# Kernel tuning notes

Measured on AMD Instinct MI355X. Metric: run time of the kernel, lower is better.

## Reference

```python
import jax, jax.numpy as jnp
import numpy as np

EPS = 1e-5

def _conv(x, w, stride=1, padding=0):
    return jax.lax.conv_general_dilated(
        x, w, window_strides=(stride, stride),
        padding=((padding, padding), (padding, padding)),
        dimension_numbers=('NCHW', 'OIHW', 'NCHW'))

def _bn(x, gamma, beta, mean, var):
    # inference-mode batchnorm, per-channel over NCHW
    inv = gamma / jnp.sqrt(var + EPS)
    return x * inv[None, :, None, None] + (beta - mean * inv)[None, :, None, None]

def setup_inputs() -> dict:
    key = jax.random.key(0)
    ks = jax.random.split(key, 16)
    B, Cin, H, W = 64, 1024, 28, 28
    width, Cout = 256, 1024
    d = {}
    d['x'] = jax.random.normal(ks[0], (B, Cin, H, W), jnp.float32)
    d['w1'] = jax.random.normal(ks[1], (width, Cin, 1, 1), jnp.float32) * 0.03
    d['w2'] = jax.random.normal(ks[2], (width, width, 3, 3), jnp.float32) * 0.02
    d['w3'] = jax.random.normal(ks[3], (Cout, width, 1, 1), jnp.float32) * 0.03
    for i, c in [(1, width), (2, width), (3, Cout)]:
        d[f'g{i}'] = jnp.ones((c,), jnp.float32)
        d[f'b{i}'] = jnp.zeros((c,), jnp.float32)
        d[f'm{i}'] = jax.random.normal(ks[4 + i], (c,), jnp.float32) * 0.1
        d[f'v{i}'] = jax.random.uniform(ks[8 + i], (c,), jnp.float32, 0.5, 1.5)
    return d

def reference(x, w1, w2, w3, g1, b1, m1, v1, g2, b2, m2, v2, g3, b3, m3, v3):
    out = jax.nn.relu(_bn(_conv(x, w1), g1, b1, m1, v1))
    out = jax.nn.relu(_bn(_conv(out, w2, stride=1, padding=1), g2, b2, m2, v2))
    out = _bn(_conv(out, w3), g3, b3, m3, v3)
    return jax.nn.relu(out + x)
```

## Files before the change

kernel.cpp:

```cpp
#include <hip/hip_runtime.h>
#include <hip/hip_bf16.h>
#include <cstdint>
#include <cstddef>

#define EPS_BN 1e-5f
#define LDK 40
#define TILE (128 * LDK)

typedef __attribute__((ext_vector_type(8))) __bf16 bf16x8;
typedef __attribute__((ext_vector_type(4))) float f32x4;

__device__ __forceinline__ unsigned short f2b(float f) {
    __hip_bfloat16 h = __float2bfloat16(f);
    return __builtin_bit_cast(unsigned short, h);
}
__device__ __forceinline__ unsigned int pack2(float a, float b) {
    return (unsigned int)f2b(a) | ((unsigned int)f2b(b) << 16);
}
__device__ __forceinline__ void lgkm_barrier() {
    __builtin_amdgcn_s_waitcnt(0xC07F);
    __builtin_amdgcn_s_barrier();
}


__global__ void prep_bn_kernel(const float* __restrict__ g1, const float* __restrict__ b1,
                               const float* __restrict__ m1, const float* __restrict__ v1,
                               const float* __restrict__ g2, const float* __restrict__ b2,
                               const float* __restrict__ m2, const float* __restrict__ v2,
                               const float* __restrict__ g3, const float* __restrict__ b3,
                               const float* __restrict__ m3, const float* __restrict__ v3,
                               float* __restrict__ bias1, float* __restrict__ bias2,
                               float* __restrict__ bias3) {
    int t = blockIdx.x * 256 + threadIdx.x;
    if (t < 256) {
        float inv = g1[t] * rsqrtf(v1[t] + EPS_BN);
        bias1[t] = b1[t] - m1[t] * inv;
    } else if (t < 512) {
        int c = t - 256;
        float inv = g2[c] * rsqrtf(v2[c] + EPS_BN);
        bias2[c] = b2[c] - m2[c] * inv;
    } else if (t < 1536) {
        int c = t - 512;
        float inv = g3[c] * rsqrtf(v3[c] + EPS_BN);
        bias3[c] = b3[c] - m3[c] * inv;
    }
}

__global__ void repack_w1(const float* __restrict__ w1, const float* __restrict__ g1,
                          const float* __restrict__ v1, unsigned short* __restrict__ w1b) {
    int idx = blockIdx.x * 256 + threadIdx.x;
    int co = idx >> 10;
    float inv = g1[co] * rsqrtf(v1[co] + EPS_BN);
    w1b[idx] = f2b(w1[idx] * inv);
}

__global__ void repack_w2(const float* __restrict__ w2, const float* __restrict__ g2,
                          const float* __restrict__ v2, unsigned short* __restrict__ w2r) {
    int idx = blockIdx.x * 256 + threadIdx.x;
    int k9 = idx >> 16;
    int rem = idx & 65535;
    int co = rem >> 8;
    int ci = rem & 255;
    float inv = g2[co] * rsqrtf(v2[co] + EPS_BN);
    w2r[idx] = f2b(w2[(co * 256 + ci) * 9 + k9] * inv);
}

__global__ void repack_w3(const float* __restrict__ w3, const float* __restrict__ g3,
                          const float* __restrict__ v3, unsigned short* __restrict__ w3b) {
    int idx = blockIdx.x * 256 + threadIdx.x;
    int co = idx >> 8;
    float inv = g3[co] * rsqrtf(v3[co] + EPS_BN);
    w3b[idx] = f2b(w3[idx] * inv);
}

__global__ void halo_zero(unsigned short* __restrict__ in2p) {
    int idx = blockIdx.x * 256 + threadIdx.x;
    int cell = idx >> 5, l8 = idx & 31;
    int n = cell / 116, c = cell % 116;
    int h, w;
    if (c < 30)      { h = 0;      w = c; }
    else if (c < 60) { h = 29;     w = c - 30; }
    else if (c < 88) { h = c - 59; w = 0; }
    else             { h = c - 87; w = 29; }
    uint4 z = {0u, 0u, 0u, 0u};
    *reinterpret_cast<uint4*>(in2p + (((size_t)n * 900) + h * 30 + w) * 256 + l8 * 8) = z;
}

__global__ __launch_bounds__(256) void transpose_x(const float* __restrict__ x,
                                                   unsigned short* __restrict__ xt) {
    __shared__ float t[64][65];
    const int tid = threadIdx.x;
    const int sp0 = blockIdx.x * 64;
    const int c0 = blockIdx.y * 64;
    const int n = blockIdx.z;
    const float* xn = x + (size_t)n * 1024 * 784;

#pragma unroll
    for (int it = 0; it < 4; ++it) {
        int ci = it * 16 + (tid >> 4);
        int spl = (tid & 15) * 4;
        int sp = sp0 + spl;
        float4 v = {0.f, 0.f, 0.f, 0.f};
        if (sp < 784) v = *reinterpret_cast<const float4*>(xn + (size_t)(c0 + ci) * 784 + sp);
        t[ci][spl + 0] = v.x;
        t[ci][spl + 1] = v.y;
        t[ci][spl + 2] = v.z;
        t[ci][spl + 3] = v.w;
    }
    __syncthreads();

    unsigned short* xtn = xt + (size_t)n * 784 * 1024;
#pragma unroll
    for (int it = 0; it < 2; ++it) {
        int spl = it * 32 + (tid >> 3);
        int sp = sp0 + spl;
        if (sp >= 784) continue;
        int ci8 = (tid & 7) * 8;
        float v0 = t[ci8 + 0][spl], v1 = t[ci8 + 1][spl];
        float v2 = t[ci8 + 2][spl], v3 = t[ci8 + 3][spl];
        float v4 = t[ci8 + 4][spl], v5 = t[ci8 + 5][spl];
        float v6 = t[ci8 + 6][spl], v7 = t[ci8 + 7][spl];
        uint4 o = {pack2(v0, v1), pack2(v2, v3), pack2(v4, v5), pack2(v6, v7)};
        *reinterpret_cast<uint4*>(xtn + (size_t)sp * 1024 + c0 + ci8) = o;
    }
}

__device__ __forceinline__ void mfma_step(const unsigned short* As, const unsigned short* Bs,
                                          int aoff, int boff, f32x4 acc[4][4]) {
    bf16x8 a[4], b[4];
#pragma unroll
    for (int i = 0; i < 4; ++i)
        a[i] = *reinterpret_cast<const bf16x8*>(As + aoff + i * 16 * LDK);
#pragma unroll
    for (int j = 0; j < 4; ++j)
        b[j] = *reinterpret_cast<const bf16x8*>(Bs + boff + j * 16 * LDK);
#pragma unroll
    for (int i = 0; i < 4; ++i)
#pragma unroll
        for (int j = 0; j < 4; ++j)
            acc[i][j] = __builtin_amdgcn_mfma_f32_16x16x32_bf16(a[i], b[j], acc[i][j], 0, 0, 0);
}

__global__ __launch_bounds__(256) void conv1_kernel(const unsigned short* __restrict__ xt,
                                                    const unsigned short* __restrict__ w1b,
                                                    const float* __restrict__ bias1,
                                                    unsigned short* __restrict__ in2p) {
    __shared__ unsigned short As[2][TILE];
    __shared__ unsigned short Bs[2][TILE];
    const int tid = threadIdx.x;
    const int f0 = blockIdx.x * 128;
    const int m0 = blockIdx.y * 128;
    const int lane = tid & 63, wave = tid >> 6;
    const int wr = wave >> 1, wc = wave & 1;
    const int l15 = lane & 15, quad = lane >> 4;
    const int tcid = tid & 3, tcl = tid >> 2;

    const unsigned short* aptr = w1b + (size_t)(m0 + tcl) * 1024 + tcid * 8;
    const unsigned short* bptr = xt + (size_t)(f0 + tcl) * 1024 + tcid * 8;

    f32x4 acc[4][4] = {};
    const int aoff = (wr * 64 + l15) * LDK + quad * 8;
    const int boff = (wc * 64 + l15) * LDK + quad * 8;
    const int wo = tcl * LDK + tcid * 8;

    uint4 ra0, ra1, rb0, rb1;
    ra0 = *reinterpret_cast<const uint4*>(aptr);
    ra1 = *reinterpret_cast<const uint4*>(aptr + 65536);
    rb0 = *reinterpret_cast<const uint4*>(bptr);
    rb1 = *reinterpret_cast<const uint4*>(bptr + 65536);

    for (int kk = 0; kk < 32; ++kk) {
        unsigned short* A = As[kk & 1];
        unsigned short* B = Bs[kk & 1];
        *reinterpret_cast<uint4*>(A + wo) = ra0;
        *reinterpret_cast<uint4*>(A + 64 * LDK + wo) = ra1;
        *reinterpret_cast<uint4*>(B + wo) = rb0;
        *reinterpret_cast<uint4*>(B + 64 * LDK + wo) = rb1;
        if (kk < 31) {
            int k0 = (kk + 1) * 32;
            ra0 = *reinterpret_cast<const uint4*>(aptr + k0);
            ra1 = *reinterpret_cast<const uint4*>(aptr + 65536 + k0);
            rb0 = *reinterpret_cast<const uint4*>(bptr + k0);
            rb1 = *reinterpret_cast<const uint4*>(bptr + 65536 + k0);
        }
        lgkm_barrier();
        mfma_step(A, B, aoff, boff, acc);
    }

#pragma unroll
    for (int j = 0; j < 4; ++j) {
        int f = f0 + wc * 64 + j * 16 + l15;
        int n = f / 784;
        int r = f - n * 784;
        int oh = r / 28, ow = r - oh * 28;
        unsigned short* dst = in2p + ((size_t)n * 900 + (oh + 1) * 30 + (ow + 1)) * 256;
#pragma unroll
        for (int i = 0; i < 4; ++i) {
            int co = m0 + wr * 64 + i * 16 + quad * 4;
            float4 bia = *reinterpret_cast<const float4*>(bias1 + co);
            f32x4 v = acc[i][j];
            ushort4 o;
            o.x = f2b(fmaxf(v.x + bia.x, 0.f));
            o.y = f2b(fmaxf(v.y + bia.y, 0.f));
            o.z = f2b(fmaxf(v.z + bia.z, 0.f));
            o.w = f2b(fmaxf(v.w + bia.w, 0.f));
            *reinterpret_cast<ushort4*>(dst + co) = o;
        }
    }
}

__global__ __launch_bounds__(256) void conv2_kernel(const unsigned short* __restrict__ in2p,
                                                    const unsigned short* __restrict__ w2r,
                                                    const float* __restrict__ bias2,
                                                    unsigned short* __restrict__ in3) {
    __shared__ unsigned short As[2][TILE];
    __shared__ unsigned short Bs[2][TILE];
    const int tid = threadIdx.x;
    const int f0 = blockIdx.x * 128;
    const int m0 = blockIdx.y * 128;
    const int lane = tid & 63, wave = tid >> 6;
    const int wr = wave >> 1, wc = wave & 1;
    const int l15 = lane & 15, quad = lane >> 4;
    const int tcid = tid & 3, tcl = tid >> 2;

    int cellc[2];
#pragma unroll
    for (int p = 0; p < 2; ++p) {
        int f = f0 + p * 64 + tcl;
        int n = f / 784;
        int r = f - n * 784;
        int oh = r / 28, ow = r - oh * 28;
        cellc[p] = n * 900 + (oh + 1) * 30 + (ow + 1);
    }

    f32x4 acc[4][4] = {};
    const int aoff = (wr * 64 + l15) * LDK + quad * 8;
    const int boff = (wc * 64 + l15) * LDK + quad * 8;
    const int wo = tcl * LDK + tcid * 8;

    uint4 ra0, ra1, rb0, rb1;
    {
        const unsigned short* wb = w2r;
        ra0 = *reinterpret_cast<const uint4*>(wb + (size_t)(m0 + tcl) * 256 + tcid * 8);
        ra1 = *reinterpret_cast<const uint4*>(wb + (size_t)(m0 + 64 + tcl) * 256 + tcid * 8);
        int dd = -31;
        rb0 = *reinterpret_cast<const uint4*>(in2p + (size_t)(cellc[0] + dd) * 256 + tcid * 8);
        rb1 = *reinterpret_cast<const uint4*>(in2p + (size_t)(cellc[1] + dd) * 256 + tcid * 8);
    }

    for (int kk = 0; kk < 72; ++kk) {
        unsigned short* A = As[kk & 1];
        unsigned short* B = Bs[kk & 1];
        *reinterpret_cast<uint4*>(A + wo) = ra0;
        *reinterpret_cast<uint4*>(A + 64 * LDK + wo) = ra1;
        *reinterpret_cast<uint4*>(B + wo) = rb0;
        *reinterpret_cast<uint4*>(B + 64 * LDK + wo) = rb1;
        if (kk < 71) {
            int kn = kk + 1;
            int k9 = kn >> 3, cb = kn & 7;
            int kh = k9 / 3, kw = k9 - 3 * kh;
            int dd = (kh - 1) * 30 + (kw - 1);
            const unsigned short* wb = w2r + (size_t)k9 * 65536 + cb * 32;
            ra0 = *reinterpret_cast<const uint4*>(wb + (size_t)(m0 + tcl) * 256 + tcid * 8);
            ra1 = *reinterpret_cast<const uint4*>(wb + (size_t)(m0 + 64 + tcl) * 256 + tcid * 8);
            const unsigned short* bb = in2p + (size_t)cb * 32 + tcid * 8;
            rb0 = *reinterpret_cast<const uint4*>(bb + (size_t)(cellc[0] + dd) * 256);
            rb1 = *reinterpret_cast<const uint4*>(bb + (size_t)(cellc[1] + dd) * 256);
        }
        lgkm_barrier();
        mfma_step(A, B, aoff, boff, acc);
    }

#pragma unroll
    for (int j = 0; j < 4; ++j) {
        int f = f0 + wc * 64 + j * 16 + l15;
        unsigned short* dst = in3 + (size_t)f * 256;
#pragma unroll
        for (int i = 0; i < 4; ++i) {
            int co = m0 + wr * 64 + i * 16 + quad * 4;
            float4 bia = *reinterpret_cast<const float4*>(bias2 + co);
            f32x4 v = acc[i][j];
            ushort4 o;
            o.x = f2b(fmaxf(v.x + bia.x, 0.f));
            o.y = f2b(fmaxf(v.y + bia.y, 0.f));
            o.z = f2b(fmaxf(v.z + bia.z, 0.f));
            o.w = f2b(fmaxf(v.w + bia.w, 0.f));
            *reinterpret_cast<ushort4*>(dst + co) = o;
        }
    }
}

__global__ __launch_bounds__(256) void conv3_kernel(const unsigned short* __restrict__ in3,
                                                    const unsigned short* __restrict__ w3b,
                                                    const float* __restrict__ bias3,
                                                    const float* __restrict__ x,
                                                    float* __restrict__ out) {
    __shared__ unsigned short As[2][TILE];
    __shared__ unsigned short Bs[2][TILE];
    const int tid = threadIdx.x;
    const int f0 = blockIdx.x * 128;
    const int m0 = blockIdx.y * 128;
    const int lane = tid & 63, wave = tid >> 6;
    const int wr = wave >> 1, wc = wave & 1;
    const int l15 = lane & 15, quad = lane >> 4;
    const int tcid = tid & 3, tcl = tid >> 2;

    const unsigned short* aptr = in3 + (size_t)(f0 + tcl) * 256 + tcid * 8;
    const unsigned short* bptr = w3b + (size_t)(m0 + tcl) * 256 + tcid * 8;

    f32x4 acc[4][4] = {};
    const int aoff = (wr * 64 + l15) * LDK + quad * 8;
    const int boff = (wc * 64 + l15) * LDK + quad * 8;
    const int wo = tcl * LDK + tcid * 8;

    uint4 ra0, ra1, rb0, rb1;
    ra0 = *reinterpret_cast<const uint4*>(aptr);
    ra1 = *reinterpret_cast<const uint4*>(aptr + 16384);
    rb0 = *reinterpret_cast<const uint4*>(bptr);
    rb1 = *reinterpret_cast<const uint4*>(bptr + 16384);

    for (int kk = 0; kk < 8; ++kk) {
        unsigned short* A = As[kk & 1];
        unsigned short* B = Bs[kk & 1];
        *reinterpret_cast<uint4*>(A + wo) = ra0;
        *reinterpret_cast<uint4*>(A + 64 * LDK + wo) = ra1;
        *reinterpret_cast<uint4*>(B + wo) = rb0;
        *reinterpret_cast<uint4*>(B + 64 * LDK + wo) = rb1;
        if (kk < 7) {
            int k0 = (kk + 1) * 32;
            ra0 = *reinterpret_cast<const uint4*>(aptr + k0);
            ra1 = *reinterpret_cast<const uint4*>(aptr + 16384 + k0);
            rb0 = *reinterpret_cast<const uint4*>(bptr + k0);
            rb1 = *reinterpret_cast<const uint4*>(bptr + 16384 + k0);
        }
        lgkm_barrier();
        mfma_step(A, B, aoff, boff, acc);
    }

#pragma unroll
    for (int j = 0; j < 4; ++j) {
        int co = m0 + wc * 64 + j * 16 + l15;
        float b = bias3[co];
#pragma unroll
        for (int i = 0; i < 4; ++i) {
            int fb = f0 + wr * 64 + i * 16 + quad * 4;
            int n = fb / 784;
            int sp = fb - n * 784;
            size_t off = ((size_t)n * 1024 + co) * 784 + sp;
            float4 xv = *reinterpret_cast<const float4*>(x + off);
            f32x4 v = acc[i][j];
            float4 o;
            o.x = fmaxf(v.x + b + xv.x, 0.f);
            o.y = fmaxf(v.y + b + xv.y, 0.f);
            o.z = fmaxf(v.z + b + xv.z, 0.f);
            o.w = fmaxf(v.w + b + xv.w, 0.f);
            *reinterpret_cast<float4*>(out + off) = o;
        }
    }
}


extern "C" void kernel_launch(void* const* d_in, const int* in_sizes, int n_in,
                              void* d_out, int out_size, void* d_ws, size_t ws_size,
                              hipStream_t stream) {
    const float* x  = (const float*)d_in[0];
    const float* w1 = (const float*)d_in[1];
    const float* w2 = (const float*)d_in[2];
    const float* w3 = (const float*)d_in[3];
    const float* g1 = (const float*)d_in[4];
    const float* b1 = (const float*)d_in[5];
    const float* m1 = (const float*)d_in[6];
    const float* v1 = (const float*)d_in[7];
    const float* g2 = (const float*)d_in[8];
    const float* b2 = (const float*)d_in[9];
    const float* m2 = (const float*)d_in[10];
    const float* v2 = (const float*)d_in[11];
    const float* g3 = (const float*)d_in[12];
    const float* b3 = (const float*)d_in[13];
    const float* m3 = (const float*)d_in[14];
    const float* v3 = (const float*)d_in[15];

    char* ws = (char*)d_ws;
    unsigned short* w1b  = (unsigned short*)(ws + 0);
    unsigned short* w2r  = (unsigned short*)(ws + 524288);
    unsigned short* w3b  = (unsigned short*)(ws + 1703936);
    float* bias1         = (float*)(ws + 2228224);
    float* bias2         = (float*)(ws + 2229248);
    float* bias3         = (float*)(ws + 2230272);
    unsigned short* in2p = (unsigned short*)(ws + 2234368);
    unsigned short* xt   = (unsigned short*)(ws + 31725568);
    unsigned short* in3  = xt;

    prep_bn_kernel<<<6, 256, 0, stream>>>(g1, b1, m1, v1, g2, b2, m2, v2, g3, b3, m3, v3,
                                          bias1, bias2, bias3);
    repack_w1<<<1024, 256, 0, stream>>>(w1, g1, v1, w1b);
    repack_w2<<<2304, 256, 0, stream>>>(w2, g2, v2, w2r);
    repack_w3<<<1024, 256, 0, stream>>>(w3, g3, v3, w3b);
    halo_zero<<<928, 256, 0, stream>>>(in2p);

    transpose_x<<<dim3(13, 16, 64), 256, 0, stream>>>(x, xt);
    conv1_kernel<<<dim3(392, 2), 256, 0, stream>>>(xt, w1b, bias1, in2p);
    conv2_kernel<<<dim3(392, 2), 256, 0, stream>>>(in2p, w2r, bias2, in3);
    conv3_kernel<<<dim3(392, 8), 256, 0, stream>>>(in3, w3b, bias3, x, (float*)d_out);
}
```

Baseline: 677.8 us.

## Stage GEMM tiles via direct global-to-LDS loads and preload residual into accumulators

```diff
diff --git a/kernel.cpp b/kernel.cpp
--- a/kernel.cpp
+++ b/kernel.cpp
@@ -4,7 +4,7 @@
 #include <cstddef>
 
 #define EPS_BN 1e-5f
-#define LDK 40
+#define LDK 32
 #define TILE (128 * LDK)
 
 typedef __attribute__((ext_vector_type(8))) __bf16 bf16x8;
@@ -17,9 +17,14 @@
 __device__ __forceinline__ unsigned int pack2(float a, float b) {
     return (unsigned int)f2b(a) | ((unsigned int)f2b(b) << 16);
 }
-__device__ __forceinline__ void lgkm_barrier() {
-    __builtin_amdgcn_s_waitcnt(0xC07F);
+__device__ __forceinline__ void vm_barrier() {
+    __builtin_amdgcn_s_waitcnt(0x3F70);
     __builtin_amdgcn_s_barrier();
+}
+__device__ __forceinline__ void load_lds16(const unsigned short* g, unsigned short* l) {
+    __builtin_amdgcn_global_load_lds(
+        (__attribute__((address_space(1))) void*)g,
+        (__attribute__((address_space(3))) void*)l, 16, 0, 0);
 }
 
 
@@ -141,6 +146,7 @@
             acc[i][j] = __builtin_amdgcn_mfma_f32_16x16x32_bf16(a[i], b[j], acc[i][j], 0, 0, 0);
 }
 
+
 __global__ __launch_bounds__(256) void conv1_kernel(const unsigned short* __restrict__ xt,
                                                     const unsigned short* __restrict__ w1b,
                                                     const float* __restrict__ bias1,
@@ -153,39 +159,32 @@
     const int lane = tid & 63, wave = tid >> 6;
     const int wr = wave >> 1, wc = wave & 1;
     const int l15 = lane & 15, quad = lane >> 4;
-    const int tcid = tid & 3, tcl = tid >> 2;
-
-    const unsigned short* aptr = w1b + (size_t)(m0 + tcl) * 1024 + tcid * 8;
-    const unsigned short* bptr = xt + (size_t)(f0 + tcl) * 1024 + tcid * 8;
+    const int srow = wave * 16 + (lane >> 2);
+    const int scol8 = (lane & 3) * 8;
+    const int lso = wave * 512;
+
+    const unsigned short* ga = w1b + (size_t)(m0 + srow) * 1024 + scol8;
+    const unsigned short* gb = xt + (size_t)(f0 + srow) * 1024 + scol8;
 
     f32x4 acc[4][4] = {};
     const int aoff = (wr * 64 + l15) * LDK + quad * 8;
     const int boff = (wc * 64 + l15) * LDK + quad * 8;
-    const int wo = tcl * LDK + tcid * 8;
-
-    uint4 ra0, ra1, rb0, rb1;
-    ra0 = *reinterpret_cast<const uint4*>(aptr);
-    ra1 = *reinterpret_cast<const uint4*>(aptr + 65536);
-    rb0 = *reinterpret_cast<const uint4*>(bptr);
-    rb1 = *reinterpret_cast<const uint4*>(bptr + 65536);
-
+
+#define STAGE1(cur, k0) do { \
+        load_lds16(ga + (k0), &As[cur][lso]); \
+        load_lds16(ga + 65536 + (k0), &As[cur][lso + 2048]); \
+        load_lds16(gb + (k0), &Bs[cur][lso]); \
+        load_lds16(gb + 65536 + (k0), &Bs[cur][lso + 2048]); \
+    } while (0)
+
+    STAGE1(0, 0);
+    vm_barrier();
     for (int kk = 0; kk < 32; ++kk) {
-        unsigned short* A = As[kk & 1];
-        unsigned short* B = Bs[kk & 1];
-        *reinterpret_cast<uint4*>(A + wo) = ra0;
-        *reinterpret_cast<uint4*>(A + 64 * LDK + wo) = ra1;
-        *reinterpret_cast<uint4*>(B + wo) = rb0;
-        *reinterpret_cast<uint4*>(B + 64 * LDK + wo) = rb1;
-        if (kk < 31) {
-            int k0 = (kk + 1) * 32;
-            ra0 = *reinterpret_cast<const uint4*>(aptr + k0);
-            ra1 = *reinterpret_cast<const uint4*>(aptr + 65536 + k0);
-            rb0 = *reinterpret_cast<const uint4*>(bptr + k0);
-            rb1 = *reinterpret_cast<const uint4*>(bptr + 65536 + k0);
-        }
-        lgkm_barrier();
-        mfma_step(A, B, aoff, boff, acc);
-    }
+        if (kk < 31) STAGE1((kk + 1) & 1, (kk + 1) * 32);
+        mfma_step(As[kk & 1], Bs[kk & 1], aoff, boff, acc);
+        vm_barrier();
+    }
+#undef STAGE1
 
 #pragma unroll
     for (int j = 0; j < 4; ++j) {
@@ -221,55 +220,46 @@
     const int lane = tid & 63, wave = tid >> 6;
     const int wr = wave >> 1, wc = wave & 1;
     const int l15 = lane & 15, quad = lane >> 4;
-    const int tcid = tid & 3, tcl = tid >> 2;
-
-    int cellc[2];
+    const int srow = wave * 16 + (lane >> 2);
+    const int scol8 = (lane & 3) * 8;
+    const int lso = wave * 512;
+
+    int cellr[2];
 #pragma unroll
     for (int p = 0; p < 2; ++p) {
-        int f = f0 + p * 64 + tcl;
+        int f = f0 + p * 64 + srow;
         int n = f / 784;
         int r = f - n * 784;
         int oh = r / 28, ow = r - oh * 28;
-        cellc[p] = n * 900 + (oh + 1) * 30 + (ow + 1);
-    }
+        cellr[p] = n * 900 + (oh + 1) * 30 + (ow + 1);
+    }
+
+    const unsigned short* wbase = w2r + (size_t)(m0 + srow) * 256 + scol8;
 
     f32x4 acc[4][4] = {};
     const int aoff = (wr * 64 + l15) * LDK + quad * 8;
     const int boff = (wc * 64 + l15) * LDK + quad * 8;
-    const int wo = tcl * LDK + tcid * 8;
-
-    uint4 ra0, ra1, rb0, rb1;
-    {
-        const unsigned short* wb = w2r;
-        ra0 = *reinterpret_cast<const uint4*>(wb + (size_t)(m0 + tcl) * 256 + tcid * 8);
-        ra1 = *reinterpret_cast<const uint4*>(wb + (size_t)(m0 + 64 + tcl) * 256 + tcid * 8);
-        int dd = -31;
-        rb0 = *reinterpret_cast<const uint4*>(in2p + (size_t)(cellc[0] + dd) * 256 + tcid * 8);
-        rb1 = *reinterpret_cast<const uint4*>(in2p + (size_t)(cellc[1] + dd) * 256 + tcid * 8);
-    }
-
+
+#define STAGE2(cur, kn) do { \
+        int k9_ = (kn) >> 3, cb_ = (kn) & 7; \
+        int kh_ = k9_ / 3, kw_ = k9_ - 3 * kh_; \
+        int dd_ = (kh_ - 1) * 30 + (kw_ - 1); \
+        const unsigned short* wa_ = wbase + (size_t)k9_ * 65536 + cb_ * 32; \
+        load_lds16(wa_, &As[cur][lso]); \
+        load_lds16(wa_ + 16384, &As[cur][lso + 2048]); \
+        const unsigned short* bb_ = in2p + (size_t)cb_ * 32 + scol8; \
+        load_lds16(bb_ + (size_t)(cellr[0] + dd_) * 256, &Bs[cur][lso]); \
+        load_lds16(bb_ + (size_t)(cellr[1] + dd_) * 256, &Bs[cur][lso + 2048]); \
+    } while (0)
+
+    STAGE2(0, 0);
+    vm_barrier();
     for (int kk = 0; kk < 72; ++kk) {
-        unsigned short* A = As[kk & 1];
-        unsigned short* B = Bs[kk & 1];
-        *reinterpret_cast<uint4*>(A + wo) = ra0;
-        *reinterpret_cast<uint4*>(A + 64 * LDK + wo) = ra1;
-        *reinterpret_cast<uint4*>(B + wo) = rb0;
-        *reinterpret_cast<uint4*>(B + 64 * LDK + wo) = rb1;
-        if (kk < 71) {
-            int kn = kk + 1;
-            int k9 = kn >> 3, cb = kn & 7;
-            int kh = k9 / 3, kw = k9 - 3 * kh;
-            int dd = (kh - 1) * 30 + (kw - 1);
-            const unsigned short* wb = w2r + (size_t)k9 * 65536 + cb * 32;
-            ra0 = *reinterpret_cast<const uint4*>(wb + (size_t)(m0 + tcl) * 256 + tcid * 8);
-            ra1 = *reinterpret_cast<const uint4*>(wb + (size_t)(m0 + 64 + tcl) * 256 + tcid * 8);
-            const unsigned short* bb = in2p + (size_t)cb * 32 + tcid * 8;
-            rb0 = *reinterpret_cast<const uint4*>(bb + (size_t)(cellc[0] + dd) * 256);
-            rb1 = *reinterpret_cast<const uint4*>(bb + (size_t)(cellc[1] + dd) * 256);
-        }
-        lgkm_barrier();
-        mfma_step(A, B, aoff, boff, acc);
-    }
+        if (kk < 71) STAGE2((kk + 1) & 1, kk + 1);
+        mfma_step(As[kk & 1], Bs[kk & 1], aoff, boff, acc);
+        vm_barrier();
+    }
+#undef STAGE2
 
 #pragma unroll
     for (int j = 0; j < 4; ++j) {
@@ -303,57 +293,68 @@
     const int lane = tid & 63, wave = tid >> 6;
     const int wr = wave >> 1, wc = wave & 1;
     const int l15 = lane & 15, quad = lane >> 4;
-    const int tcid = tid & 3, tcl = tid >> 2;
-
-    const unsigned short* aptr = in3 + (size_t)(f0 + tcl) * 256 + tcid * 8;
-    const unsigned short* bptr = w3b + (size_t)(m0 + tcl) * 256 + tcid * 8;
-
-    f32x4 acc[4][4] = {};
+    const int srow = wave * 16 + (lane >> 2);
+    const int scol8 = (lane & 3) * 8;
+    const int lso = wave * 512;
+
+    const unsigned short* ga = in3 + (size_t)(f0 + srow) * 256 + scol8;
+    const unsigned short* gb = w3b + (size_t)(m0 + srow) * 256 + scol8;
+
     const int aoff = (wr * 64 + l15) * LDK + quad * 8;
     const int boff = (wc * 64 + l15) * LDK + quad * 8;
-    const int wo = tcl * LDK + tcid * 8;
-
-    uint4 ra0, ra1, rb0, rb1;
-    ra0 = *reinterpret_cast<const uint4*>(aptr);
-    ra1 = *reinterpret_cast<const uint4*>(aptr + 16384);
-    rb0 = *reinterpret_cast<const uint4*>(bptr);
-    rb1 = *reinterpret_cast<const uint4*>(bptr + 16384);
-
-    for (int kk = 0; kk < 8; ++kk) {
-        unsigned short* A = As[kk & 1];
-        unsigned short* B = Bs[kk & 1];
-        *reinterpret_cast<uint4*>(A + wo) = ra0;
-        *reinterpret_cast<uint4*>(A + 64 * LDK + wo) = ra1;
-        *reinterpret_cast<uint4*>(B + wo) = rb0;
-        *reinterpret_cast<uint4*>(B + 64 * LDK + wo) = rb1;
-        if (kk < 7) {
-            int k0 = (kk + 1) * 32;
-            ra0 = *reinterpret_cast<const uint4*>(aptr + k0);
-            ra1 = *reinterpret_cast<const uint4*>(aptr + 16384 + k0);
-            rb0 = *reinterpret_cast<const uint4*>(bptr + k0);
-            rb1 = *reinterpret_cast<const uint4*>(bptr + 16384 + k0);
-        }
-        lgkm_barrier();
-        mfma_step(A, B, aoff, boff, acc);
-    }
-
+
+#define STAGE3(cur, k0) do { \
+        load_lds16(ga + (k0), &As[cur][lso]); \
+        load_lds16(ga + 16384 + (k0), &As[cur][lso + 2048]); \
+        load_lds16(gb + (k0), &Bs[cur][lso]); \
+        load_lds16(gb + 16384 + (k0), &Bs[cur][lso + 2048]); \
+    } while (0)
+
+    STAGE3(0, 0);
+
+    f32x4 acc[4][4];
 #pragma unroll
     for (int j = 0; j < 4; ++j) {
         int co = m0 + wc * 64 + j * 16 + l15;
         float b = bias3[co];
+#pragma unroll
+        for (int i = 0; i < 4; ++i) {
+            int fb = f0 + wr * 64 + i * 16 + quad * 4;
+            int n = fb / 784;
+            int sp = fb - n * 784;
+            float4 xr = *reinterpret_cast<const float4*>(x + ((size_t)n * 1024 + co) * 784 + sp);
+            f32x4 a;
+            a.x = xr.x + b;
+            a.y = xr.y + b;
+            a.z = xr.z + b;
+            a.w = xr.w + b;
+            acc[i][j] = a;
+        }
+    }
+
+    vm_barrier();
+    for (int kk = 0; kk < 8; ++kk) {
+        if (kk < 7) STAGE3((kk + 1) & 1, (kk + 1) * 32);
+        mfma_step(As[kk & 1], Bs[kk & 1], aoff, boff, acc);
+        vm_barrier();
+    }
+#undef STAGE3
+
+#pragma unroll
+    for (int j = 0; j < 4; ++j) {
+        int co = m0 + wc * 64 + j * 16 + l15;
 #pragma unroll
         for (int i = 0; i < 4; ++i) {
             int fb = f0 + wr * 64 + i * 16 + quad * 4;
             int n = fb / 784;
             int sp = fb - n * 784;
             size_t off = ((size_t)n * 1024 + co) * 784 + sp;
-            float4 xv = *reinterpret_cast<const float4*>(x + off);
             f32x4 v = acc[i][j];
             float4 o;
-            o.x = fmaxf(v.x + b + xv.x, 0.f);
-            o.y = fmaxf(v.y + b + xv.y, 0.f);
-            o.z = fmaxf(v.z + b + xv.z, 0.f);
-            o.w = fmaxf(v.w + b + xv.w, 0.f);
+            o.x = fmaxf(v.x, 0.f);
+            o.y = fmaxf(v.y, 0.f);
+            o.z = fmaxf(v.z, 0.f);
+            o.w = fmaxf(v.w, 0.f);
             *reinterpret_cast<float4*>(out + off) = o;
         }
     }
```

New measurement: 680.3 us. Within noise of the previous version (+0.4%).
